# Kernel optimization log

Measured on AMD Instinct MI355X. Metric: run time of the kernel, lower is better.

The kernel has to match this reference:

```python
import jax, jax.numpy as jnp
import numpy as np

N = 8192
F_IN = 128
D = 128
NEG_SLOPE = 0.2  # cfg.negativeslope (standard GAT value)
MASK_FILL = -9e15


def setup_inputs() -> dict:
    key = jax.random.key(0)
    k1, k2, k3, k4 = jax.random.split(key, 4)
    A = jax.random.randint(k1, (N, N), 0, 2, dtype=jnp.int32)
    X = jax.random.normal(k2, (N, F_IN), dtype=jnp.float32)
    # glorot init for Ws, xavier_uniform(gain=1.414) for a
    lim_w = float(np.sqrt(6.0 / (F_IN + D)))
    Ws = jax.random.uniform(k3, (F_IN, D), minval=-lim_w, maxval=lim_w, dtype=jnp.float32)
    lim_a = 1.414 * float(np.sqrt(6.0 / (2 * D + 1)))
    a = jax.random.uniform(k4, (2 * D, 1), minval=-lim_a, maxval=lim_a, dtype=jnp.float32)
    return {"A": A, "X": X, "Ws": Ws, "a": a}


def reference(A, X, Ws, a):
    # Wh: [N, D]
    Wh = X @ Ws
    d = Wh.shape[-1]
    # additive attention: e_ij = leaky_relu(Wh_i . a1 + Wh_j . a2)
    e1 = Wh @ a[:d]          # [N, 1]
    e2 = Wh @ a[d:]          # [N, 1]
    e = jax.nn.leaky_relu(e1 + e2.T, negative_slope=NEG_SLOPE)  # [N, N]
    e = jnp.where(A > 0, e, MASK_FILL)
    attn = jax.nn.softmax(e, axis=1)  # row-wise over neighbors
    H = attn @ Wh            # [N, D]
    return H
```

## Files before the change

kernel.cpp:

```cpp
#include <hip/hip_runtime.h>
#include <hip/hip_bf16.h>

#define NN 8192
#define DD 128

typedef __attribute__((ext_vector_type(8))) short short8;
typedef __attribute__((ext_vector_type(4))) float f32x4;
typedef unsigned int u32;

__device__ __forceinline__ ushort f2bf(float f) {
    __hip_bfloat16 h = __float2bfloat16(f);
    return *(ushort*)&h;
}
__device__ __forceinline__ float asf(u32 u) {
    union { u32 i; float f; } v; v.i = u; return v.f;
}

__device__ __forceinline__ void async_ld16(const void* g, void* l) {
    __builtin_amdgcn_global_load_lds(
        (const __attribute__((address_space(1))) u32*)g,
        (__attribute__((address_space(3))) u32*)l, 16, 0, 0);
}

__global__ __launch_bounds__(256) void k1_fused(
    const float* __restrict__ X, const float* __restrict__ Ws,
    const float* __restrict__ a, ushort* __restrict__ WhT,
    float* __restrict__ C1, float* __restrict__ C1s, u32* __restrict__ E2bf) {
    __shared__ float lWs[128 * 132];
    __shared__ float lX[32 * 132];
    __shared__ float la[256];
    int t = threadIdx.x, bx = blockIdx.x;
    int i0 = bx * 32;
    const float4* Ws4 = (const float4*)Ws;
    const float4* X4 = (const float4*)X;
    la[t] = a[t];
    for (int j = 0; j < 16; ++j) {
        int u = j * 256 + t;
        int k = u >> 5, c4 = u & 31;
        *(float4*)&lWs[k * 132 + c4 * 4] = Ws4[u];
    }
    for (int j = 0; j < 4; ++j) {
        int u = j * 256 + t;
        int r = u >> 5, c4 = u & 31;
        *(float4*)&lX[r * 132 + c4 * 4] = X4[bx * 1024 + u];
    }
    __syncthreads();
    int r0 = (t >> 5) * 4, c0 = (t & 31) * 4;
    float acc[4][4];
#pragma unroll
    for (int i = 0; i < 4; ++i)
#pragma unroll
        for (int j = 0; j < 4; ++j) acc[i][j] = 0.f;
#pragma unroll 4
    for (int k = 0; k < 128; ++k) {
        float4 wv = *(const float4*)&lWs[k * 132 + c0];
        float x0 = lX[(r0 + 0) * 132 + k];
        float x1 = lX[(r0 + 1) * 132 + k];
        float x2 = lX[(r0 + 2) * 132 + k];
        float x3 = lX[(r0 + 3) * 132 + k];
#pragma unroll
        for (int j = 0; j < 4; ++j) {
            acc[0][j] += x0 * ((const float*)&wv)[j];
            acc[1][j] += x1 * ((const float*)&wv)[j];
            acc[2][j] += x2 * ((const float*)&wv)[j];
            acc[3][j] += x3 * ((const float*)&wv)[j];
        }
    }
    __syncthreads();
    float* lT = lWs;
#pragma unroll
    for (int i = 0; i < 4; ++i)
#pragma unroll
        for (int j = 0; j < 4; ++j) lT[(c0 + j) * 33 + r0 + i] = acc[i][j];
    __syncthreads();
    if (t < 128) {
        int r = t >> 2, q = t & 3;
        float s1 = 0.f, s2 = 0.f;
        for (int j = 0; j < 32; ++j) {
            int d = q * 32 + j;
            float v = lT[d * 33 + r];
            s1 += v * la[d];
            s2 += v * la[128 + d];
        }
        s1 += __shfl_xor(s1, 1); s1 += __shfl_xor(s1, 2);
        s2 += __shfl_xor(s2, 1); s2 += __shfl_xor(s2, 2);
        if (q == 0) {
            int i = i0 + r;
            C1[i]  = __expf(s1);
            C1s[i] = __expf(0.2f * s1);
            u32 pe = (u32)f2bf(__expf(s2));
            u32 ne = (u32)f2bf(__expf(0.2f * s2));
            E2bf[i] = pe | (ne << 16);
        }
    }
    int d = t >> 1, hf = t & 1;
    __attribute__((aligned(16))) ushort tmp[16];
#pragma unroll
    for (int s = 0; s < 16; ++s) tmp[s] = f2bf(lT[d * 33 + hf * 16 + s]);
    uint4* dst = (uint4*)&WhT[(size_t)d * NN + i0 + hf * 16];
    const uint4* srcv = (const uint4*)tmp;
    dst[0] = srcv[0];
    dst[1] = srcv[1];
}

__global__ __launch_bounds__(1024, 8) void k3_main(
    const int* __restrict__ A, const ushort* __restrict__ WhT,
    const float* __restrict__ C1, const float* __restrict__ C1s,
    const u32* __restrict__ E2bf, float* __restrict__ Hp,
    float* __restrict__ Lp) {

    __shared__ __align__(16) ushort lB[2][16][64][8];
    __shared__ u32 lE[2048];

    int tid = threadIdx.x;
    int lane = tid & 63;
    int wv = tid >> 6;
    int g = wv & 3;
    int h = wv >> 2;
    int n = lane & 15;
    int kg = lane >> 4;

    int bx = blockIdx.x;
    int kb = blockIdx.y;
    int row = bx * 64 + g * 16 + n;
    int kbase = kb * 2048;

    lE[tid] = E2bf[kbase + tid];
    lE[tid + 1024] = E2bf[kbase + tid + 1024];

    float c1 = C1[row], c1s = C1s[row];
    const int* Arow = A + (size_t)row * NN + kbase + kg * 8;

    int cc_s = wv & 7, tp_s = wv >> 3;
    const ushort* srcB = WhT + (size_t)(cc_s * 16 + n) * NN + kbase + tp_s * 32 + kg * 8;
    ushort* dstB0 = &lB[0][cc_s * 2 + tp_s][lane][0];
    ushort* dstB1 = &lB[1][cc_s * 2 + tp_s][lane][0];

    short8 ones;
#pragma unroll
    for (int j = 0; j < 8; ++j) ones[j] = (short)0x3F80;

    f32x4 acc0 = (f32x4){0.f, 0.f, 0.f, 0.f};
    f32x4 acc1 = (f32x4){0.f, 0.f, 0.f, 0.f};
    f32x4 accl = (f32x4){0.f, 0.f, 0.f, 0.f};

    async_ld16(srcB, dstB0);
    __syncthreads();

    for (int kt = 0; kt < 32; ++kt) {
        int b = kt & 1;
        const int* Ak = Arow + kt * 64;
        int4 a00 = *(const int4*)(Ak);
        int4 a01 = *(const int4*)(Ak + 4);
        int4 a10 = *(const int4*)(Ak + 32);
        int4 a11 = *(const int4*)(Ak + 36);
        if (kt < 31)
            async_ld16(srcB + (kt + 1) * 64, b ? dstB0 : dstB1);
#pragma unroll
        for (int tp = 0; tp < 2; ++tp) {
            int ke = kt * 64 + tp * 32 + kg * 8;
            uint4 e0 = *(const uint4*)&lE[ke];
            uint4 e1 = *(const uint4*)&lE[ke + 4];
            int am[8];
            *(int4*)(am) = tp ? a10 : a00;
            *(int4*)(am + 4) = tp ? a11 : a01;
            u32 ev[8];
            *(uint4*)(ev) = e0; *(uint4*)(ev + 4) = e1;
            short8 af;
#pragma unroll
            for (int u = 0; u < 8; ++u) {
                float ep = asf(ev[u] << 16);
                float en = asf(ev[u] & 0xFFFF0000u);
                float w = fmaxf(c1 * ep, c1s * en);
                w = am[u] ? w : 0.f;
                af[u] = (short)f2bf(w);
            }
            short8 b0 = *(const short8*)&lB[b][(2 * h + 0) * 2 + tp][lane][0];
            short8 b1 = *(const short8*)&lB[b][(2 * h + 1) * 2 + tp][lane][0];
            acc0 = __builtin_amdgcn_mfma_f32_16x16x32_bf16(af, b0, acc0, 0, 0, 0);
            acc1 = __builtin_amdgcn_mfma_f32_16x16x32_bf16(af, b1, acc1, 0, 0, 0);
            accl = __builtin_amdgcn_mfma_f32_16x16x32_bf16(af, ones, accl, 0, 0, 0);
        }
        __syncthreads();
    }

    if (h == 0 && n == 0) {
#pragma unroll
        for (int r = 0; r < 4; ++r)
            Lp[(size_t)kb * NN + bx * 64 + g * 16 + kg * 4 + r] = accl[r];
    }
    float* Hpb = Hp + (size_t)kb * (NN * DD);
#pragma unroll
    for (int r = 0; r < 4; ++r) {
        int orow = bx * 64 + g * 16 + kg * 4 + r;
        Hpb[(size_t)orow * DD + h * 32 + n] = acc0[r];
        Hpb[(size_t)orow * DD + h * 32 + 16 + n] = acc1[r];
    }
}

__global__ void k4_final(const float* __restrict__ Hp, const float* __restrict__ Lp,
                         float* __restrict__ out) {
    int idx = blockIdx.x * 256 + threadIdx.x;
    int i = idx >> 7;
    float sv = Hp[idx] + Hp[1048576 + idx] + Hp[2097152 + idx] + Hp[3145728 + idx];
    float l = Lp[i] + Lp[8192 + i] + Lp[16384 + i] + Lp[24576 + i];
    out[idx] = sv / l;
}

extern "C" void kernel_launch(void* const* d_in, const int* in_sizes, int n_in,
                              void* d_out, int out_size, void* d_ws, size_t ws_size,
                              hipStream_t stream) {
    const int*   A  = (const int*)d_in[0];
    const float* X  = (const float*)d_in[1];
    const float* Ws = (const float*)d_in[2];
    const float* a  = (const float*)d_in[3];
    float* out = (float*)d_out;

    char* ws = (char*)d_ws;
    ushort* WhT  = (ushort*)(ws);
    float*  C1   = (float*)(ws + (2u << 20));
    float*  C1s  = (float*)(ws + (2u << 20) + (32u << 10));
    u32*    E2bf = (u32*)(ws + (2u << 20) + (64u << 10));
    float*  Lp   = (float*)(ws + (2u << 20) + (96u << 10));
    float*  Hp   = (float*)(ws + (4u << 20));

    k1_fused<<<256, 256, 0, stream>>>(X, Ws, a, WhT, C1, C1s, E2bf);
    k3_main<<<dim3(128, 4), 1024, 0, stream>>>(A, WhT, C1, C1s, E2bf, Hp, Lp);
    k4_final<<<4096, 256, 0, stream>>>(Hp, Lp, out);
}
```

Before: 463.8 us.

## Load WhT B-fragments directly to registers, halve block size, prefetch A rows

The main attention-aggregation kernel drops its LDS double-buffered async staging of WhT and its per-iteration barriers. Each wave now loads its B fragments straight from global into registers and covers 64 output columns with four accumulators. Blocks shrink from 1024 to 512 threads, the adjacency-mask int4 loads are software-pipelined one tile ahead, and the bf16 packing uses a byte-permute that truncates instead of rounding. Only half the waves compute the row-sum MFMA. This removes barrier stalls and LDS traffic, at the cost of redundant global/L2 reads of WhT across waves and higher register pressure.

```diff
diff --git a/kernel.cpp b/kernel.cpp
--- a/kernel.cpp
+++ b/kernel.cpp
@@ -15,11 +15,8 @@
 __device__ __forceinline__ float asf(u32 u) {
     union { u32 i; float f; } v; v.i = u; return v.f;
 }
-
-__device__ __forceinline__ void async_ld16(const void* g, void* l) {
-    __builtin_amdgcn_global_load_lds(
-        (const __attribute__((address_space(1))) u32*)g,
-        (__attribute__((address_space(3))) u32*)l, 16, 0, 0);
+__device__ __forceinline__ u32 asu(float f) {
+    union { float f; u32 i; } v; v.f = f; return v.i;
 }
 
 __global__ __launch_bounds__(256) void k1_fused(
@@ -103,13 +100,12 @@
     dst[1] = srcv[1];
 }
 
-__global__ __launch_bounds__(1024, 8) void k3_main(
+__global__ __launch_bounds__(512, 4) void k3_main(
     const int* __restrict__ A, const ushort* __restrict__ WhT,
     const float* __restrict__ C1, const float* __restrict__ C1s,
     const u32* __restrict__ E2bf, float* __restrict__ Hp,
     float* __restrict__ Lp) {
 
-    __shared__ __align__(16) ushort lB[2][16][64][8];
     __shared__ u32 lE[2048];
 
     int tid = threadIdx.x;
@@ -125,16 +121,15 @@
     int row = bx * 64 + g * 16 + n;
     int kbase = kb * 2048;
 
-    lE[tid] = E2bf[kbase + tid];
-    lE[tid + 1024] = E2bf[kbase + tid + 1024];
+#pragma unroll
+    for (int j = 0; j < 4; ++j) lE[tid + j * 512] = E2bf[kbase + tid + j * 512];
 
     float c1 = C1[row], c1s = C1s[row];
     const int* Arow = A + (size_t)row * NN + kbase + kg * 8;
-
-    int cc_s = wv & 7, tp_s = wv >> 3;
-    const ushort* srcB = WhT + (size_t)(cc_s * 16 + n) * NN + kbase + tp_s * 32 + kg * 8;
-    ushort* dstB0 = &lB[0][cc_s * 2 + tp_s][lane][0];
-    ushort* dstB1 = &lB[1][cc_s * 2 + tp_s][lane][0];
+    const ushort* Bc0 = WhT + (size_t)(h * 64 +  0 + n) * NN + kbase + kg * 8;
+    const ushort* Bc1 = WhT + (size_t)(h * 64 + 16 + n) * NN + kbase + kg * 8;
+    const ushort* Bc2 = WhT + (size_t)(h * 64 + 32 + n) * NN + kbase + kg * 8;
+    const ushort* Bc3 = WhT + (size_t)(h * 64 + 48 + n) * NN + kbase + kg * 8;
 
     short8 ones;
 #pragma unroll
@@ -142,46 +137,65 @@
 
     f32x4 acc0 = (f32x4){0.f, 0.f, 0.f, 0.f};
     f32x4 acc1 = (f32x4){0.f, 0.f, 0.f, 0.f};
+    f32x4 acc2 = (f32x4){0.f, 0.f, 0.f, 0.f};
+    f32x4 acc3 = (f32x4){0.f, 0.f, 0.f, 0.f};
     f32x4 accl = (f32x4){0.f, 0.f, 0.f, 0.f};
 
-    async_ld16(srcB, dstB0);
-    __syncthreads();
-
+    __syncthreads();
+
+    int4 Ar[2][4];
+    Ar[0][0] = *(const int4*)(Arow);
+    Ar[0][1] = *(const int4*)(Arow + 4);
+    Ar[0][2] = *(const int4*)(Arow + 32);
+    Ar[0][3] = *(const int4*)(Arow + 36);
+
+#pragma unroll 2
     for (int kt = 0; kt < 32; ++kt) {
         int b = kt & 1;
-        const int* Ak = Arow + kt * 64;
-        int4 a00 = *(const int4*)(Ak);
-        int4 a01 = *(const int4*)(Ak + 4);
-        int4 a10 = *(const int4*)(Ak + 32);
-        int4 a11 = *(const int4*)(Ak + 36);
-        if (kt < 31)
-            async_ld16(srcB + (kt + 1) * 64, b ? dstB0 : dstB1);
+        int ko = kt * 64;
+        short8 B00 = *(const short8*)(Bc0 + ko);
+        short8 B10 = *(const short8*)(Bc1 + ko);
+        short8 B20 = *(const short8*)(Bc2 + ko);
+        short8 B30 = *(const short8*)(Bc3 + ko);
+        short8 B01 = *(const short8*)(Bc0 + ko + 32);
+        short8 B11 = *(const short8*)(Bc1 + ko + 32);
+        short8 B21 = *(const short8*)(Bc2 + ko + 32);
+        short8 B31 = *(const short8*)(Bc3 + ko + 32);
+        if (kt < 31) {
+            Ar[b ^ 1][0] = *(const int4*)(Arow + ko + 64);
+            Ar[b ^ 1][1] = *(const int4*)(Arow + ko + 68);
+            Ar[b ^ 1][2] = *(const int4*)(Arow + ko + 96);
+            Ar[b ^ 1][3] = *(const int4*)(Arow + ko + 100);
+        }
 #pragma unroll
         for (int tp = 0; tp < 2; ++tp) {
-            int ke = kt * 64 + tp * 32 + kg * 8;
+            int ke = ko + tp * 32 + kg * 8;
             uint4 e0 = *(const uint4*)&lE[ke];
             uint4 e1 = *(const uint4*)&lE[ke + 4];
-            int am[8];
-            *(int4*)(am) = tp ? a10 : a00;
-            *(int4*)(am + 4) = tp ? a11 : a01;
-            u32 ev[8];
+            int am[8]; u32 ev[8];
+            *(int4*)(am) = Ar[b][tp * 2];
+            *(int4*)(am + 4) = Ar[b][tp * 2 + 1];
             *(uint4*)(ev) = e0; *(uint4*)(ev + 4) = e1;
-            short8 af;
+            u32 wb[8];
 #pragma unroll
             for (int u = 0; u < 8; ++u) {
                 float ep = asf(ev[u] << 16);
                 float en = asf(ev[u] & 0xFFFF0000u);
                 float w = fmaxf(c1 * ep, c1s * en);
                 w = am[u] ? w : 0.f;
-                af[u] = (short)f2bf(w);
+                wb[u] = asu(w);
             }
-            short8 b0 = *(const short8*)&lB[b][(2 * h + 0) * 2 + tp][lane][0];
-            short8 b1 = *(const short8*)&lB[b][(2 * h + 1) * 2 + tp][lane][0];
-            acc0 = __builtin_amdgcn_mfma_f32_16x16x32_bf16(af, b0, acc0, 0, 0, 0);
-            acc1 = __builtin_amdgcn_mfma_f32_16x16x32_bf16(af, b1, acc1, 0, 0, 0);
-            accl = __builtin_amdgcn_mfma_f32_16x16x32_bf16(af, ones, accl, 0, 0, 0);
-        }
-        __syncthreads();
+            short8 af;
+#pragma unroll
+            for (int p = 0; p < 4; ++p)
+                ((u32*)&af)[p] = __builtin_amdgcn_perm(wb[2 * p + 1], wb[2 * p], 0x07060302);
+            acc0 = __builtin_amdgcn_mfma_f32_16x16x32_bf16(af, tp ? B01 : B00, acc0, 0, 0, 0);
+            acc1 = __builtin_amdgcn_mfma_f32_16x16x32_bf16(af, tp ? B11 : B10, acc1, 0, 0, 0);
+            acc2 = __builtin_amdgcn_mfma_f32_16x16x32_bf16(af, tp ? B21 : B20, acc2, 0, 0, 0);
+            acc3 = __builtin_amdgcn_mfma_f32_16x16x32_bf16(af, tp ? B31 : B30, acc3, 0, 0, 0);
+            if (h == 0)
+                accl = __builtin_amdgcn_mfma_f32_16x16x32_bf16(af, ones, accl, 0, 0, 0);
+        }
     }
 
     if (h == 0 && n == 0) {
@@ -193,8 +207,10 @@
 #pragma unroll
     for (int r = 0; r < 4; ++r) {
         int orow = bx * 64 + g * 16 + kg * 4 + r;
-        Hpb[(size_t)orow * DD + h * 32 + n] = acc0[r];
-        Hpb[(size_t)orow * DD + h * 32 + 16 + n] = acc1[r];
+        Hpb[(size_t)orow * DD + h * 64 + n]      = acc0[r];
+        Hpb[(size_t)orow * DD + h * 64 + 16 + n] = acc1[r];
+        Hpb[(size_t)orow * DD + h * 64 + 32 + n] = acc2[r];
+        Hpb[(size_t)orow * DD + h * 64 + 48 + n] = acc3[r];
     }
 }
 
@@ -225,6 +241,6 @@
     float*  Hp   = (float*)(ws + (4u << 20));
 
     k1_fused<<<256, 256, 0, stream>>>(X, Ws, a, WhT, C1, C1s, E2bf);
-    k3_main<<<dim3(128, 4), 1024, 0, stream>>>(A, WhT, C1, C1s, E2bf, Hp, Lp);
+    k3_main<<<dim3(128, 4), 512, 0, stream>>>(A, WhT, C1, C1s, E2bf, Hp, Lp);
     k4_final<<<4096, 256, 0, stream>>>(Hp, Lp, out);
 }
```

Result: slower. 476.0 us (+2.6%).
